# Kernel optimization log

Hardware: AMD Instinct MI355X
Metric: run time of the kernel (lower is better)

Reference implementation:

```python
import jax, jax.numpy as jnp
from jax import lax
import numpy as np

N, BITS, NCLS = 2048, 64, 100
LAMBDA = 1.0
ALPHA = 1.0


def setup_inputs() -> dict:
    key = jax.random.key(0)
    ku, kl = jax.random.split(key)
    u = jax.random.normal(ku, (N, BITS), dtype=jnp.float32)
    labels = jax.random.randint(kl, (N,), 0, NCLS)
    y = jax.nn.one_hot(labels, NCLS, dtype=jnp.float32)  # [N, C]
    return {"u": u, "y": y}


def reference(u, y):
    # inner_product[i, j] = <u_i, u_j>;  s[i, j] = (y_i . y_j > 0)
    ip = u @ u.T                      # [N, N]
    s = (y @ y.T) > 0                 # [N, N] bool

    def step(carry, xs):
        tot, cnt = carry
        ip_row, s_row = xs            # [N], [N]
        pos = s_row
        neg = ~s_row
        # triple[p, n] = ip[p] - ip[n] - ALPHA, clamped like the original
        T = jnp.clip(ip_row[:, None] - ip_row[None, :] - ALPHA, -100.0, 50.0)
        # -(T - log(1 + exp(T))) = softplus(T) - T
        L = jax.nn.softplus(T) - T    # [N, N]
        pm = (pos[:, None] & neg[None, :]).astype(L.dtype)
        npairs = pm.sum()
        valid = (pos.sum() > 0) & (neg.sum() > 0)
        row_loss = jnp.where(valid, (L * pm).sum() / jnp.maximum(npairs, 1.0), 0.0)
        return (tot + row_loss, cnt + valid.astype(jnp.float32)), None

    (tot, cnt), _ = lax.scan(step, (jnp.float32(0.0), jnp.float32(0.0)), (ip, s))
    loss1 = jnp.where(cnt > 0, tot / jnp.maximum(cnt, 1.0), 0.0)
    loss2 = LAMBDA * jnp.mean((u - jnp.sign(u)) ** 2)
    return loss1 + loss2
```

## Files before the change

kernel.cpp:

```cpp
#include <hip/hip_runtime.h>
#include <math.h>

#define NROWS 2048
#define BITS  64
#define NCLS  100
#define ALPHA_C  1.0f
#define LAMBDA_C 1.0f
#define ECLAMP   1.8e19f


__device__ __forceinline__ float block_reduce_sum(float v, float* wsum) {
    __syncthreads();
    #pragma unroll
    for (int off = 32; off > 0; off >>= 1) v += __shfl_down(v, off);
    int tid = threadIdx.x;
    if ((tid & 63) == 0) wsum[tid >> 6] = v;
    __syncthreads();
    float r = 0.f;
    if (tid == 0) {
        #pragma unroll
        for (int w = 0; w < 4; ++w) r += wsum[w];
    }
    return r;
}

__device__ __forceinline__ float softplus_mt(float T) {
    return fmaxf(-T, 0.f) + __logf(1.f + __expf(-fabsf(T)));
}


#define TJ  256
#define SJT 257

__global__ __launch_bounds__(256) void combo_kernel(const float* __restrict__ u,
                                                    const float* __restrict__ y,
                                                    float* __restrict__ G,
                                                    unsigned char* __restrict__ lab8,
                                                    float* __restrict__ quantp) {
    __shared__ float ujT[64 * SJT];
    __shared__ float uiT[64 * 8];
    __shared__ float wsum[4];
    const int tid = threadIdx.x;

    if (blockIdx.x < 512) {
        const int ig = blockIdx.x >> 1;
        const int jh = blockIdx.x & 1;
        const int i0 = ig * 8;
        const int jb = jh * 1024;

        float qs = 0.f;
        if (jh == 0) {
            #pragma unroll
            for (int t = tid; t < 8 * BITS; t += 256) {
                float v = u[(size_t)i0 * BITS + t];
                float sg = (v > 0.f) ? 1.f : ((v < 0.f) ? -1.f : 0.f);
                float d = v - sg;
                qs = fmaf(d, d, qs);
            }
        }

        #pragma unroll
        for (int it = 0; it < 2; ++it) {
            const int flat = tid + it * 256;
            const int r = flat >> 6, k = flat & 63;
            uiT[k * 8 + r] = u[(size_t)i0 * BITS + flat];
        }
        if (jh == 0) {
            float qt = block_reduce_sum(qs, wsum);
            if (tid == 0) quantp[ig] = qt;
        }
        __syncthreads();

        for (int jt = 0; jt < 1024 / TJ; ++jt) {
            const int j0 = jb + jt * TJ;
            #pragma unroll
            for (int it = 0; it < 16; ++it) {
                const int flat = tid + it * 256;
                const int r = flat >> 4, q = flat & 15;
                float4 v = *(const float4*)(u + (size_t)(j0 + r) * BITS + q * 4);
                ujT[(4 * q + 0) * SJT + r] = v.x;
                ujT[(4 * q + 1) * SJT + r] = v.y;
                ujT[(4 * q + 2) * SJT + r] = v.z;
                ujT[(4 * q + 3) * SJT + r] = v.w;
            }
            __syncthreads();

            float acc[8];
            #pragma unroll
            for (int r = 0; r < 8; ++r) acc[r] = 0.f;
            #pragma unroll 4
            for (int k = 0; k < BITS; ++k) {
                const float e = ujT[k * SJT + tid];
                const float4 w0 = *(const float4*)&uiT[k * 8 + 0];
                const float4 w1 = *(const float4*)&uiT[k * 8 + 4];
                acc[0] = fmaf(w0.x, e, acc[0]);
                acc[1] = fmaf(w0.y, e, acc[1]);
                acc[2] = fmaf(w0.z, e, acc[2]);
                acc[3] = fmaf(w0.w, e, acc[3]);
                acc[4] = fmaf(w1.x, e, acc[4]);
                acc[5] = fmaf(w1.y, e, acc[5]);
                acc[6] = fmaf(w1.z, e, acc[6]);
                acc[7] = fmaf(w1.w, e, acc[7]);
            }
            #pragma unroll
            for (int r = 0; r < 8; ++r)
                G[(size_t)(i0 + r) * NROWS + j0 + tid] = acc[r];
            __syncthreads();
        }
    } else {
        const int bi = blockIdx.x - 512;
        const int row = bi * 4 + (tid >> 6);
        const int lane = tid & 63;
        const float* yr = y + (size_t)row * NCLS;
        float v0 = yr[lane];
        float v1 = (lane < NCLS - 64) ? yr[lane + 64] : 0.f;
        unsigned long long m0 = __ballot(v0 > 0.5f);
        unsigned long long m1 = __ballot(v1 > 0.5f);
        if (lane == 0) {
            int c = m0 ? (__ffsll(m0) - 1) : (m1 ? 64 + __ffsll(m1) - 1 : 0);
            lab8[row] = (unsigned char)c;
        }
    }
}

__global__ __launch_bounds__(256, 4) void eval2_kernel(const float* __restrict__ G,
                                                       const unsigned char* __restrict__ lab8,
                                                       float* __restrict__ rl,
                                                       float* __restrict__ vl) {
    alignas(16) __shared__ float ap0[NROWS + 8];
    alignas(16) __shared__ float ap1[NROWS + 8];
    __shared__ int np0_s, np1_s;
    __shared__ float w0s[4], w1s[4];
    const int i0 = blockIdx.x * 2, i1 = i0 + 1;
    const int tid = threadIdx.x;
    if (tid == 0) { np0_s = 0; np1_s = 0; }
    __syncthreads();
    const int c0 = lab8[i0];
    const int c1 = lab8[i1];

    float av0[8], av1[8];
    int lv[8];
    {
        const float4* g04 = (const float4*)(G + (size_t)i0 * NROWS) + tid * 2;
        const float4* g14 = (const float4*)(G + (size_t)i1 * NROWS) + tid * 2;
        float4 a0 = g04[0], a1 = g04[1];
        float4 b0 = g14[0], b1 = g14[1];
        av0[0] = a0.x; av0[1] = a0.y; av0[2] = a0.z; av0[3] = a0.w;
        av0[4] = a1.x; av0[5] = a1.y; av0[6] = a1.z; av0[7] = a1.w;
        av1[0] = b0.x; av1[1] = b0.y; av1[2] = b0.z; av1[3] = b0.w;
        av1[4] = b1.x; av1[5] = b1.y; av1[6] = b1.z; av1[7] = b1.w;
        uint2 lw = *(const uint2*)(lab8 + (size_t)tid * 8);
        #pragma unroll
        for (int m = 0; m < 4; ++m) lv[m] = (lw.x >> (8 * m)) & 0xFF;
        #pragma unroll
        for (int m = 0; m < 4; ++m) lv[4 + m] = (lw.y >> (8 * m)) & 0xFF;
    }

    float Eb0[8], Eb1[8];
    #pragma unroll
    for (int m = 0; m < 8; ++m) {
        const bool p0 = (lv[m] == c0);
        const bool p1 = (lv[m] == c1);
        if (p0) { int k = atomicAdd(&np0_s, 1); ap0[k] = fminf(__expf(-av0[m]), ECLAMP); }
        if (p1) { int k = atomicAdd(&np1_s, 1); ap1[k] = fminf(__expf(-av1[m]), ECLAMP); }
        Eb0[m] = p0 ? 0.f : fminf(__expf(av0[m] + ALPHA_C), ECLAMP);
        Eb1[m] = p1 ? 0.f : fminf(__expf(av1[m] + ALPHA_C), ECLAMP);
    }
    __syncthreads();
    const int np0 = np0_s, np1 = np1_s;
    const int npr = (((np0 > np1) ? np0 : np1) + 3) & ~3;
    for (int k = np0 + tid; k < npr; k += 256) ap0[k] = 0.f;
    for (int k = np1 + tid; k < npr; k += 256) ap1[k] = 0.f;
    __syncthreads();

    float s0 = 0.f, s1 = 0.f, s2 = 0.f, s3 = 0.f;
    float t0 = 0.f, t1 = 0.f, t2 = 0.f, t3 = 0.f;
    for (int k = 0; k < npr; k += 4) {
        const float4 e0 = *(const float4*)(ap0 + k);
        const float4 e1 = *(const float4*)(ap1 + k);
        #pragma unroll
        for (int m = 0; m < 8; ++m) {
            const float q0 = Eb0[m], q1 = Eb1[m];
            s0 += __log2f(fmaf(q0, e0.x, 1.f));
            s1 += __log2f(fmaf(q0, e0.y, 1.f));
            s2 += __log2f(fmaf(q0, e0.z, 1.f));
            s3 += __log2f(fmaf(q0, e0.w, 1.f));
            t0 += __log2f(fmaf(q1, e1.x, 1.f));
            t1 += __log2f(fmaf(q1, e1.y, 1.f));
            t2 += __log2f(fmaf(q1, e1.z, 1.f));
            t3 += __log2f(fmaf(q1, e1.w, 1.f));
        }
    }

    float r0 = (s0 + s1) + (s2 + s3);
    float r1 = (t0 + t1) + (t2 + t3);
    #pragma unroll
    for (int off = 32; off > 0; off >>= 1) {
        r0 += __shfl_down(r0, off);
        r1 += __shfl_down(r1, off);
    }
    if ((tid & 63) == 0) { w0s[tid >> 6] = r0; w1s[tid >> 6] = r1; }
    __syncthreads();
    if (tid == 0) {
        const float ln2 = 0.6931471805599453f;
        float tot0 = (w0s[0] + w0s[1]) + (w0s[2] + w0s[3]);
        float tot1 = (w1s[0] + w1s[1]) + (w1s[2] + w1s[3]);
        const int nneg0 = NROWS - np0, nneg1 = NROWS - np1;
        const int v0 = (np0 > 0 && nneg0 > 0) ? 1 : 0;
        const int v1 = (np1 > 0 && nneg1 > 0) ? 1 : 0;
        rl[i0] = v0 ? (tot0 * ln2 / fmaxf((float)np0 * (float)nneg0, 1.f)) : 0.f;
        rl[i1] = v1 ? (tot1 * ln2 / fmaxf((float)np1 * (float)nneg1, 1.f)) : 0.f;
        vl[i0] = (float)v0;
        vl[i1] = (float)v1;
    }
}

__global__ __launch_bounds__(256) void finalize2_kernel(const float* __restrict__ rl,
                                                        const float* __restrict__ vl,
                                                        const float* __restrict__ qp,
                                                        float* __restrict__ out) {
    __shared__ float wsum[4];
    const int tid = threadIdx.x;
    float t = 0.f, v = 0.f;
    for (int idx = tid; idx < NROWS; idx += 256) { t += rl[idx]; v += vl[idx]; }
    float q = qp[tid];
    float tt = block_reduce_sum(t, wsum);
    float vv = block_reduce_sum(v, wsum);
    float qq = block_reduce_sum(q, wsum);
    if (tid == 0) {
        const float loss1 = (vv > 0.f) ? (tt / fmaxf(vv, 1.f)) : 0.f;
        const float loss2 = LAMBDA_C * (qq / (float)(NROWS * BITS));
        out[0] = loss1 + loss2;
    }
}


__global__ __launch_bounds__(256) void labels_only_kernel(const float* __restrict__ y,
                                                          int* __restrict__ labels) {
    const int tid = threadIdx.x;
    const int row = blockIdx.x * 4 + (tid >> 6);
    const int lane = tid & 63;
    const float* yr = y + (size_t)row * NCLS;
    float v0 = yr[lane];
    float v1 = (lane < NCLS - 64) ? yr[lane + 64] : 0.f;
    unsigned long long m0 = __ballot(v0 > 0.5f);
    unsigned long long m1 = __ballot(v1 > 0.5f);
    if (lane == 0) {
        int c = m0 ? (__ffsll(m0) - 1) : (m1 ? 64 + __ffsll(m1) - 1 : 0);
        labels[row] = c;
    }
}

__global__ __launch_bounds__(256) void row_loss_kernel(const float* __restrict__ u,
                                                       const int* __restrict__ labels,
                                                       float* __restrict__ acc) {
    __shared__ float a[NROWS];
    __shared__ float apv[NROWS];
    __shared__ int lab[NROWS];
    __shared__ float ui[BITS];
    __shared__ int npos_s;
    __shared__ float wsum[4];

    const int i = blockIdx.x;
    const int tid = threadIdx.x;

    if (tid < BITS) ui[tid] = u[(size_t)i * BITS + tid];
    if (tid == 0) npos_s = 0;
    __syncthreads();

    #pragma unroll
    for (int m = 0; m < NROWS / 256; ++m) {
        const int j = tid + m * 256;
        const float4* uj = (const float4*)(u + (size_t)j * BITS);
        float s0 = 0.f, s1 = 0.f, s2 = 0.f, s3 = 0.f;
        #pragma unroll
        for (int q = 0; q < BITS / 4; ++q) {
            float4 v = uj[q];
            s0 = fmaf(v.x, ui[4 * q + 0], s0);
            s1 = fmaf(v.y, ui[4 * q + 1], s1);
            s2 = fmaf(v.z, ui[4 * q + 2], s2);
            s3 = fmaf(v.w, ui[4 * q + 3], s3);
        }
        a[j] = (s0 + s1) + (s2 + s3);
        lab[j] = labels[j];
    }
    __syncthreads();

    const int c = lab[i];
    #pragma unroll
    for (int m = 0; m < NROWS / 256; ++m) {
        const int j = tid + m * 256;
        if (lab[j] == c) { int k = atomicAdd(&npos_s, 1); apv[k] = a[j]; }
    }
    __syncthreads();
    const int npos = npos_s;
    const int nneg = NROWS - npos;

    float b[NROWS / 256];
    #pragma unroll
    for (int m = 0; m < NROWS / 256; ++m) {
        const int j = tid + m * 256;
        b[m] = (lab[j] != c) ? (a[j] + ALPHA_C) : -3.0e38f;
    }

    float lsum = 0.f;
    for (int k = 0; k < npos; ++k) {
        const float apk = apv[k];
        #pragma unroll
        for (int m = 0; m < NROWS / 256; ++m) lsum += softplus_mt(apk - b[m]);
    }

    float tot = block_reduce_sum(lsum, wsum);
    if (tid == 0) {
        const int valid = (npos > 0 && nneg > 0) ? 1 : 0;
        const float npairs = fmaxf((float)npos * (float)nneg, 1.f);
        const float rlv = valid ? (tot / npairs) : 0.f;
        atomicAdd(&acc[0], rlv);
        atomicAdd(&acc[1], (float)valid);
    }
}

__global__ __launch_bounds__(256) void quant_kernel(const float* __restrict__ u,
                                                    float* __restrict__ acc) {
    __shared__ float wsum[4];
    const int stride = gridDim.x * 256;
    float s = 0.f;
    for (int t = blockIdx.x * 256 + threadIdx.x; t < NROWS * BITS; t += stride) {
        float v = u[t];
        float sg = (v > 0.f) ? 1.f : ((v < 0.f) ? -1.f : 0.f);
        float d = v - sg;
        s = fmaf(d, d, s);
    }
    float tot = block_reduce_sum(s, wsum);
    if (threadIdx.x == 0) atomicAdd(&acc[2], tot);
}

__global__ void finalize_kernel(const float* __restrict__ acc,
                                float* __restrict__ out) {
    const float tot = acc[0], cnt = acc[1], q = acc[2];
    const float loss1 = (cnt > 0.f) ? (tot / fmaxf(cnt, 1.f)) : 0.f;
    const float loss2 = LAMBDA_C * (q / (float)(NROWS * BITS));
    out[0] = loss1 + loss2;
}


extern "C" void kernel_launch(void* const* d_in, const int* in_sizes, int n_in,
                              void* d_out, int out_size, void* d_ws, size_t ws_size,
                              hipStream_t stream) {
    const float* u = (const float*)d_in[0];
    const float* y = (const float*)d_in[1];
    float* out = (float*)d_out;

    unsigned char* lab8 = (unsigned char*)d_ws;
    float* rl = (float*)((char*)d_ws + 8192);
    float* vl = (float*)((char*)d_ws + 16384);
    float* qp = (float*)((char*)d_ws + 24576);
    float* G  = (float*)((char*)d_ws + 32768);
    const size_t NEED = 32768 + (size_t)NROWS * NROWS * sizeof(float);

    if (ws_size >= NEED) {
        combo_kernel<<<1024, 256, 0, stream>>>(u, y, G, lab8, qp);
        eval2_kernel<<<NROWS / 2, 256, 0, stream>>>(G, lab8, rl, vl);
        finalize2_kernel<<<1, 256, 0, stream>>>(rl, vl, qp, out);
    } else {
        float* acc  = (float*)d_ws;
        int*   lab2 = (int*)((char*)d_ws + 256);
        hipMemsetAsync(d_ws, 0, 256, stream);
        labels_only_kernel<<<512, 256, 0, stream>>>(y, lab2);
        row_loss_kernel<<<NROWS, 256, 0, stream>>>(u, lab2, acc);
        quant_kernel<<<64, 256, 0, stream>>>(u, acc);
        finalize_kernel<<<1, 1, 0, stream>>>(acc, out);
    }
}
```

Before: 99.77 us.

## Compute Gram matrix with bf16 MFMA after separate bf16 conversion pass

Splits the fused FP32 Gram kernel into a prep kernel and a gram kernel. The prep kernel converts u to bf16 and computes the quantization partial sums and labels. The gram kernel computes u·uᵀ with 16x16x32 bf16 MFMA instructions instead of scalar FMAs over shared-memory tiles. This cuts the matrix-multiply cost but adds a kernel launch. The bf16 inputs also perturb the inner products that feed the softplus loss, which may hurt accuracy.

Result: faster. 89.97 us (-9.8%).

```diff
diff --git a/kernel.cpp b/kernel.cpp
--- a/kernel.cpp
+++ b/kernel.cpp
@@ -1,4 +1,5 @@
 #include <hip/hip_runtime.h>
+#include <hip/hip_bf16.h>
 #include <math.h>
 
 #define NROWS 2048
@@ -8,6 +9,9 @@
 #define LAMBDA_C 1.0f
 #define ECLAMP   1.8e19f
 
+typedef __bf16 bf16x8 __attribute__((ext_vector_type(8)));
+typedef float  floatx4 __attribute__((ext_vector_type(4)));
+
 
 __device__ __forceinline__ float block_reduce_sum(float v, float* wsum) {
     __syncthreads();
@@ -29,86 +33,34 @@
 }
 
 
-#define TJ  256
-#define SJT 257
-
-__global__ __launch_bounds__(256) void combo_kernel(const float* __restrict__ u,
-                                                    const float* __restrict__ y,
-                                                    float* __restrict__ G,
-                                                    unsigned char* __restrict__ lab8,
-                                                    float* __restrict__ quantp) {
-    __shared__ float ujT[64 * SJT];
-    __shared__ float uiT[64 * 8];
-    __shared__ float wsum[4];
-    const int tid = threadIdx.x;
-
-    if (blockIdx.x < 512) {
-        const int ig = blockIdx.x >> 1;
-        const int jh = blockIdx.x & 1;
-        const int i0 = ig * 8;
-        const int jb = jh * 1024;
-
-        float qs = 0.f;
-        if (jh == 0) {
-            #pragma unroll
-            for (int t = tid; t < 8 * BITS; t += 256) {
-                float v = u[(size_t)i0 * BITS + t];
-                float sg = (v > 0.f) ? 1.f : ((v < 0.f) ? -1.f : 0.f);
-                float d = v - sg;
-                qs = fmaf(d, d, qs);
-            }
+__global__ __launch_bounds__(256) void prep_kernel(const float* __restrict__ u,
+                                                   const float* __restrict__ y,
+                                                   unsigned short* __restrict__ ub,
+                                                   unsigned char* __restrict__ lab8,
+                                                   float* __restrict__ qp) {
+    const int tid = threadIdx.x;
+    if (blockIdx.x < 64) {
+        __shared__ float wsum[4];
+        const int base = blockIdx.x * 2048 + tid * 8;
+        float4 v0 = *(const float4*)(u + base);
+        float4 v1 = *(const float4*)(u + base + 4);
+        float vv[8] = {v0.x, v0.y, v0.z, v0.w, v1.x, v1.y, v1.z, v1.w};
+        unsigned short ob[8];
+        float q = 0.f;
+        #pragma unroll
+        for (int m = 0; m < 8; ++m) {
+            const float v = vv[m];
+            const float sg = (v > 0.f) ? 1.f : ((v < 0.f) ? -1.f : 0.f);
+            const float d = v - sg;
+            q = fmaf(d, d, q);
+            __hip_bfloat16 h = __float2bfloat16(v);
+            ob[m] = *reinterpret_cast<unsigned short*>(&h);
         }
-
-        #pragma unroll
-        for (int it = 0; it < 2; ++it) {
-            const int flat = tid + it * 256;
-            const int r = flat >> 6, k = flat & 63;
-            uiT[k * 8 + r] = u[(size_t)i0 * BITS + flat];
-        }
-        if (jh == 0) {
-            float qt = block_reduce_sum(qs, wsum);
-            if (tid == 0) quantp[ig] = qt;
-        }
-        __syncthreads();
-
-        for (int jt = 0; jt < 1024 / TJ; ++jt) {
-            const int j0 = jb + jt * TJ;
-            #pragma unroll
-            for (int it = 0; it < 16; ++it) {
-                const int flat = tid + it * 256;
-                const int r = flat >> 4, q = flat & 15;
-                float4 v = *(const float4*)(u + (size_t)(j0 + r) * BITS + q * 4);
-                ujT[(4 * q + 0) * SJT + r] = v.x;
-                ujT[(4 * q + 1) * SJT + r] = v.y;
-                ujT[(4 * q + 2) * SJT + r] = v.z;
-                ujT[(4 * q + 3) * SJT + r] = v.w;
-            }
-            __syncthreads();
-
-            float acc[8];
-            #pragma unroll
-            for (int r = 0; r < 8; ++r) acc[r] = 0.f;
-            #pragma unroll 4
-            for (int k = 0; k < BITS; ++k) {
-                const float e = ujT[k * SJT + tid];
-                const float4 w0 = *(const float4*)&uiT[k * 8 + 0];
-                const float4 w1 = *(const float4*)&uiT[k * 8 + 4];
-                acc[0] = fmaf(w0.x, e, acc[0]);
-                acc[1] = fmaf(w0.y, e, acc[1]);
-                acc[2] = fmaf(w0.z, e, acc[2]);
-                acc[3] = fmaf(w0.w, e, acc[3]);
-                acc[4] = fmaf(w1.x, e, acc[4]);
-                acc[5] = fmaf(w1.y, e, acc[5]);
-                acc[6] = fmaf(w1.z, e, acc[6]);
-                acc[7] = fmaf(w1.w, e, acc[7]);
-            }
-            #pragma unroll
-            for (int r = 0; r < 8; ++r)
-                G[(size_t)(i0 + r) * NROWS + j0 + tid] = acc[r];
-            __syncthreads();
-        }
+        *(uint4*)(ub + base) = *(const uint4*)ob;
+        float t = block_reduce_sum(q, wsum);
+        if (tid == 0) qp[blockIdx.x] = t;
     } else {
-        const int bi = blockIdx.x - 512;
+        const int bi = blockIdx.x - 64;
         const int row = bi * 4 + (tid >> 6);
         const int lane = tid & 63;
         const float* yr = y + (size_t)row * NCLS;
@@ -120,6 +72,38 @@
             int c = m0 ? (__ffsll(m0) - 1) : (m1 ? 64 + __ffsll(m1) - 1 : 0);
             lab8[row] = (unsigned char)c;
         }
+    }
+}
+
+__global__ __launch_bounds__(256) void gram_kernel(const unsigned short* __restrict__ ub,
+                                                   float* __restrict__ G) {
+    const int tid  = threadIdx.x;
+    const int gw   = blockIdx.x * 4 + (tid >> 6);
+    const int lane = tid & 63;
+    const int i0   = (gw >> 5) * 16;
+    const int j0   = (gw & 31) * 64;
+    const int rsel = lane & 15;
+    const int quad = lane >> 4;
+    const int koff = quad * 8;
+
+    uint4 a0r = *(const uint4*)(ub + (size_t)(i0 + rsel) * BITS + koff);
+    uint4 a1r = *(const uint4*)(ub + (size_t)(i0 + rsel) * BITS + 32 + koff);
+    bf16x8 A0 = __builtin_bit_cast(bf16x8, a0r);
+    bf16x8 A1 = __builtin_bit_cast(bf16x8, a1r);
+
+    #pragma unroll
+    for (int s = 0; s < 4; ++s) {
+        const int jr = j0 + s * 16 + rsel;
+        uint4 b0r = *(const uint4*)(ub + (size_t)jr * BITS + koff);
+        uint4 b1r = *(const uint4*)(ub + (size_t)jr * BITS + 32 + koff);
+        bf16x8 B0 = __builtin_bit_cast(bf16x8, b0r);
+        bf16x8 B1 = __builtin_bit_cast(bf16x8, b1r);
+        floatx4 c = {0.f, 0.f, 0.f, 0.f};
+        c = __builtin_amdgcn_mfma_f32_16x16x32_bf16(A0, B0, c, 0, 0, 0);
+        c = __builtin_amdgcn_mfma_f32_16x16x32_bf16(A1, B1, c, 0, 0, 0);
+        #pragma unroll
+        for (int r = 0; r < 4; ++r)
+            G[(size_t)(i0 + quad * 4 + r) * NROWS + j0 + s * 16 + rsel] = c[r];
     }
 }
 
@@ -223,7 +207,7 @@
     const int tid = threadIdx.x;
     float t = 0.f, v = 0.f;
     for (int idx = tid; idx < NROWS; idx += 256) { t += rl[idx]; v += vl[idx]; }
-    float q = qp[tid];
+    float q = (tid < 64) ? qp[tid] : 0.f;
     float tt = block_reduce_sum(t, wsum);
     float vv = block_reduce_sum(v, wsum);
     float qq = block_reduce_sum(q, wsum);
@@ -355,11 +339,13 @@
     float* rl = (float*)((char*)d_ws + 8192);
     float* vl = (float*)((char*)d_ws + 16384);
     float* qp = (float*)((char*)d_ws + 24576);
-    float* G  = (float*)((char*)d_ws + 32768);
-    const size_t NEED = 32768 + (size_t)NROWS * NROWS * sizeof(float);
+    unsigned short* ub = (unsigned short*)((char*)d_ws + 32768);
+    float* G  = (float*)((char*)d_ws + 294912);
+    const size_t NEED = 294912 + (size_t)NROWS * NROWS * sizeof(float);
 
     if (ws_size >= NEED) {
-        combo_kernel<<<1024, 256, 0, stream>>>(u, y, G, lab8, qp);
+        prep_kernel<<<576, 256, 0, stream>>>(u, y, ub, lab8, qp);
+        gram_kernel<<<1024, 256, 0, stream>>>(ub, G);
         eval2_kernel<<<NROWS / 2, 256, 0, stream>>>(G, lab8, rl, vl);
         finalize2_kernel<<<1, 256, 0, stream>>>(rl, vl, qp, out);
     } else {
```
